# Optimization experiments

Hardware: AMD Instinct MI355X
Metric: run time of the kernel (lower is better)

Reference implementation:

```python
import jax, jax.numpy as jnp
import numpy as np

N_NODES, N_EDGES = 50000, 400000
D_IN, D_HID, D_OUT, N_LAYERS = 256, 512, 128, 4


def setup_inputs() -> dict:
    key = jax.random.key(0)
    ks = jax.random.split(key, 8)
    x = jax.random.normal(ks[0], (N_NODES, D_IN), jnp.float32)
    edge_index = jax.random.randint(ks[1], (2, N_EDGES), 0, N_NODES)
    # dnn1: Linear(D_IN, D_HID)
    W1 = jax.random.normal(ks[2], (D_IN, D_HID), jnp.float32) / np.sqrt(D_IN)
    b1 = jnp.zeros((D_HID,), jnp.float32)
    # stacked GCNConv weights: [L, D_HID, D_HID]
    Wc = jax.random.normal(ks[3], (N_LAYERS, D_HID, D_HID), jnp.float32) / np.sqrt(D_HID)
    bc = jnp.zeros((N_LAYERS, D_HID), jnp.float32)
    # dnn2: Linear(D_HID, D_OUT)
    W2 = jax.random.normal(ks[4], (D_HID, D_OUT), jnp.float32) / np.sqrt(D_HID)
    b2 = jnp.zeros((D_OUT,), jnp.float32)
    return {"x": x, "edge_index": edge_index, "W1": W1, "b1": b1,
            "Wc": Wc, "bc": bc, "W2": W2, "b2": b2}


def reference(x, edge_index, W1, b1, Wc, bc, W2, b2):
    N = x.shape[0]
    L = Wc.shape[0]
    # GCNConv: add self-loops once (same graph every layer)
    loops = jnp.arange(N, dtype=edge_index.dtype)
    src = jnp.concatenate([edge_index[0], loops])  # message sources
    dst = jnp.concatenate([edge_index[1], loops])  # message targets
    deg = jax.ops.segment_sum(jnp.ones_like(dst, dtype=x.dtype), dst, num_segments=N)
    dinv = jnp.where(deg > 0, jax.lax.rsqrt(deg), 0.0)  # deg >= 1 due to self-loops
    norm = dinv[src] * dinv[dst]                        # [E+N]

    # dnn1: Linear + ReLU
    h = jax.nn.relu(x @ W1 + b1)

    # GCN layers: h' = scatter_dst( norm * (h W)[src] ) + b
    for i in range(L):
        hw = h @ Wc[i]
        msgs = norm[:, None] * hw[src]                  # [E+N, D_HID]
        h = jax.ops.segment_sum(msgs, dst, num_segments=N) + bc[i]

    # dnn2: Linear
    return h @ W2 + b2
```

## Files before the change

kernel.cpp:

```cpp
#include <hip/hip_runtime.h>

typedef __bf16 bf16_t;
typedef __bf16 bf16x8 __attribute__((ext_vector_type(8)));
typedef float f32x4 __attribute__((ext_vector_type(4)));
typedef float f32x2 __attribute__((ext_vector_type(2)));

#define N_NODES 50000
#define N_PAD   50048
#define N_EDGES 400000
#define D_IN    256
#define D_HID   512
#define D_OUT   128
#define N_LAYERS 4
#define ZROW    N_PAD
#define CSR_CAP (N_EDGES + 3 * N_NODES + 64)
#define PZ_FLOATS (3 * 512 * 512)

#define AS1 __attribute__((address_space(1)))
#define AS3 __attribute__((address_space(3)))


__global__ void init_misc(int* __restrict__ deg, int* __restrict__ cursor,
                          int* __restrict__ csr_src, float* __restrict__ dinv,
                          float* __restrict__ u0, float* __restrict__ u1,
                          float* __restrict__ u2, bf16_t* __restrict__ FA,
                          bf16_t* __restrict__ FB, float* __restrict__ Pz) {
    int idx = blockIdx.x * blockDim.x + threadIdx.x;
    if (idx < CSR_CAP) csr_src[idx] = ZROW;
    if (idx < N_NODES) { deg[idx] = 0; cursor[idx] = 0; }
    if (idx < N_PAD - N_NODES) dinv[N_NODES + idx] = 0.0f;
    if (idx < N_PAD + 1 - N_NODES) {
        u0[N_NODES + idx] = 0.0f; u1[N_NODES + idx] = 0.0f; u2[N_NODES + idx] = 0.0f;
    }
    if (idx < 64) {
        ((unsigned*)(FA + (size_t)ZROW * D_OUT))[idx] = 0u;
        ((unsigned*)(FB + (size_t)ZROW * D_OUT))[idx] = 0u;
    }
    if (idx < PZ_FLOATS) Pz[idx] = 0.0f;
}


__global__ void f32_to_bf16(const float* __restrict__ in, bf16_t* __restrict__ out, int n) {
    int idx = (blockIdx.x * blockDim.x + threadIdx.x) * 4;
    if (idx + 3 < n) {
        float4 v = *reinterpret_cast<const float4*>(in + idx);
        bf16_t o[4] = {(bf16_t)v.x, (bf16_t)v.y, (bf16_t)v.z, (bf16_t)v.w};
        *reinterpret_cast<uint2*>(out + idx) = *reinterpret_cast<const uint2*>(o);
    } else {
        for (int j = idx; j < n; j++) out[j] = (bf16_t)in[j];
    }
}


__global__ void transpose_all(const float* __restrict__ W1, const float* __restrict__ Wc,
                              const float* __restrict__ W2, bf16_t* __restrict__ W1t,
                              float* __restrict__ W2cT, float* __restrict__ W4cT,
                              float* __restrict__ W2T) {
    const float* in; int R, C; bf16_t* outb = nullptr; float* outf = nullptr;
    const int z = blockIdx.z;
    if (z == 0)      { in = W1; R = D_IN;  C = D_HID; outb = W1t; }
    else if (z == 1) { in = Wc + (size_t)1 * D_HID * D_HID; R = D_HID; C = D_HID; outf = W2cT; }
    else if (z == 2) { in = Wc + (size_t)3 * D_HID * D_HID; R = D_HID; C = D_HID; outf = W4cT; }
    else             { in = W2; R = D_HID; C = D_OUT; outf = W2T; }

    const int c0 = blockIdx.x * 32;
    const int r0 = blockIdx.y * 32;
    if (c0 >= C || r0 >= R) return;
    __shared__ float tile[32][33];
    for (int i = threadIdx.y; i < 32; i += 8)
        tile[i][threadIdx.x] = in[(size_t)(r0 + i) * C + c0 + threadIdx.x];
    __syncthreads();
    for (int i = threadIdx.y; i < 32; i += 8) {
        if (outb) outb[(size_t)(c0 + i) * R + r0 + threadIdx.x] = (bf16_t)tile[threadIdx.x][i];
        else      outf[(size_t)(c0 + i) * R + r0 + threadIdx.x] = tile[threadIdx.x][i];
    }
}


__global__ void count_deg(const int* __restrict__ dst, int* __restrict__ deg, int E) {
    int e = blockIdx.x * blockDim.x + threadIdx.x;
    if (e < E) atomicAdd(&deg[dst[e]], 1);
}

__global__ void scan_reduce(const int* __restrict__ deg, int* __restrict__ partial, int N) {
    __shared__ int red[256];
    int base = blockIdx.x * 1024;
    int s = 0;
    for (int i = threadIdx.x; i < 1024; i += 256) {
        int idx = base + i;
        s += (idx < N) ? ((deg[idx] + 3) & ~3) : 0;
    }
    red[threadIdx.x] = s;
    __syncthreads();
    for (int off = 128; off > 0; off >>= 1) {
        if (threadIdx.x < off) red[threadIdx.x] += red[threadIdx.x + off];
        __syncthreads();
    }
    if (threadIdx.x == 0) partial[blockIdx.x] = red[0];
}

__global__ void scan_partials(int* __restrict__ partial, int nb,
                              int* __restrict__ row_start, int N) {
    if (threadIdx.x == 0 && blockIdx.x == 0) {
        int acc = 0;
        for (int i = 0; i < nb; i++) { int v = partial[i]; partial[i] = acc; acc += v; }
        row_start[N] = acc;
    }
}

__global__ void scan_chunks(const int* __restrict__ deg, const int* __restrict__ partial,
                            int* __restrict__ row_start, float* __restrict__ dinv,
                            float* __restrict__ u0, int N) {
    __shared__ int buf[2][1024];
    int t = threadIdx.x;
    int gid = blockIdx.x * 1024 + t;
    int d = (gid < N) ? deg[gid] : 0;
    int v = (gid < N) ? ((d + 3) & ~3) : 0;
    int cur = 0;
    buf[0][t] = v;
    __syncthreads();
    for (int off = 1; off < 1024; off <<= 1) {
        int nxt = cur ^ 1;
        int val = buf[cur][t];
        if (t >= off) val += buf[cur][t - off];
        buf[nxt][t] = val;
        cur = nxt;
        __syncthreads();
    }
    int incl = buf[cur][t];
    if (gid < N) {
        row_start[gid] = partial[blockIdx.x] + incl - v;
        float dv = rsqrtf((float)(d + 1));
        dinv[gid] = dv;
        u0[gid] = dv;
    }
}

__global__ void fill_csr(const int* __restrict__ ei, int E,
                         const int* __restrict__ row_start,
                         int* __restrict__ cursor, int* __restrict__ csr_src) {
    int e = blockIdx.x * blockDim.x + threadIdx.x;
    if (e < E) {
        int s = ei[e];
        int d = ei[E + e];
        int pos = atomicAdd(&cursor[d], 1);
        csr_src[row_start[d] + pos] = s;
    }
}


template <bool F32OUT, bool RELU>
__global__ __launch_bounds__(256, 4) void gemm_tile(
    const bf16_t* __restrict__ A, const bf16_t* __restrict__ BT,
    const float* __restrict__ bias, const float* __restrict__ rowscale,
    void* __restrict__ Cv, int M, int N, int K)
{
    __shared__ __align__(16) char smem[32768];
    bf16_t* sA = (bf16_t*)smem;
    bf16_t* sB = (bf16_t*)(smem + 128 * 128);
    bf16_t* sC = (bf16_t*)smem;

    int bxi, byi;
    if (gridDim.x == 4) {
        const int bid = blockIdx.y * 4 + blockIdx.x;
        const int T0 = (int)(gridDim.y * 4) & ~31;
        if (bid < T0) { int q = bid >> 5, r = bid & 31; byi = q * 8 + (r & 7); bxi = r >> 3; }
        else          { int t = bid - T0; byi = (T0 >> 2) + (t >> 2); bxi = t & 3; }
    } else { bxi = blockIdx.x; byi = blockIdx.y; }

    const int tid  = threadIdx.x;
    const int lane = tid & 63;
    const int wave = tid >> 6;
    const int bn = bxi * 128;
    const int bm = byi * 128;
    const int wm = (wave & 1) * 64;
    const int wn = (wave >> 1) * 64;
    const int lm = lane & 15;
    const int lq = lane >> 4;

    const int r8 = lane >> 3;
    const int c8 = lane & 7;
    const int ksw = (c8 ^ r8) * 8;

    f32x4 acc[4][4] = {};

    const int nkb = K >> 6;
    for (int kb = 0; kb < nkb; kb++) {
        const int k0 = kb * 64;
#pragma unroll
        for (int r = 0; r < 4; r++) {
            const int g = r * 4 + wave;
            __builtin_amdgcn_global_load_lds(
                (const AS1 unsigned int*)(A + (size_t)(bm + g * 8 + r8) * K + k0 + ksw),
                (AS3 unsigned int*)((AS3 char*)(AS3 bf16_t*)sA + g * 1024),
                16, 0, 0);
        }
#pragma unroll
        for (int r = 0; r < 4; r++) {
            const int g = r * 4 + wave;
            __builtin_amdgcn_global_load_lds(
                (const AS1 unsigned int*)(BT + (size_t)(bn + g * 8 + r8) * K + k0 + ksw),
                (AS3 unsigned int*)((AS3 char*)(AS3 bf16_t*)sB + g * 1024),
                16, 0, 0);
        }
        __syncthreads();

#pragma unroll
        for (int s = 0; s < 2; s++) {
            bf16x8 af[4], bfr[4];
#pragma unroll
            for (int mt = 0; mt < 4; mt++) {
                const int R = wm + mt * 16 + lm;
                const int g = s * 4 + lq;
                af[mt] = *reinterpret_cast<bf16x8*>(&sA[R * 64 + ((g ^ (R & 7)) * 8)]);
            }
#pragma unroll
            for (int nt = 0; nt < 4; nt++) {
                const int R = wn + nt * 16 + lm;
                const int g = s * 4 + lq;
                bfr[nt] = *reinterpret_cast<bf16x8*>(&sB[R * 64 + ((g ^ (R & 7)) * 8)]);
            }
#pragma unroll
            for (int mt = 0; mt < 4; mt++)
#pragma unroll
                for (int nt = 0; nt < 4; nt++)
                    acc[mt][nt] = __builtin_amdgcn_mfma_f32_16x16x32_bf16(af[mt], bfr[nt], acc[mt][nt], 0, 0, 0);
        }
        __syncthreads();
    }

    if (!F32OUT) {
        const size_t rowbytes = (size_t)N * 2;
#pragma unroll
        for (int p = 0; p < 2; p++) {
            if (p) __syncthreads();
            if ((wave & 1) == p) {
#pragma unroll
                for (int nt = 0; nt < 4; nt++) {
                    const int col = wn + nt * 16 + lm;
                    const float bv = bias ? bias[bn + col] : 0.0f;
#pragma unroll
                    for (int mt = 0; mt < 4; mt++) {
#pragma unroll
                        for (int r = 0; r < 4; r++) {
                            const int lrow = mt * 16 + lq * 4 + r;
                            float v = acc[mt][nt][r] + bv;
                            if (rowscale) v *= rowscale[bm + p * 64 + lrow];
                            if (RELU) v = fmaxf(v, 0.0f);
                            sC[lrow * 136 + col] = (bf16_t)v;
                        }
                    }
                }
            }
            __syncthreads();
            char* outbase = (char*)Cv + (size_t)(bm + p * 64) * rowbytes + (size_t)bn * 2;
#pragma unroll
            for (int j = 0; j < 4; j++) {
                const int idx = j * 4096 + tid * 16;
                const int row = idx >> 8;
                const int colb = idx & 255;
                *reinterpret_cast<uint4*>(outbase + (size_t)row * rowbytes + colb) =
                    *reinterpret_cast<const uint4*>((char*)sC + (size_t)row * 272 + colb);
            }
        }
    } else {
#pragma unroll
        for (int nt = 0; nt < 4; nt++) {
            const int col = bn + wn + nt * 16 + lm;
            const float bv = bias ? bias[col] : 0.0f;
#pragma unroll
            for (int mt = 0; mt < 4; mt++) {
#pragma unroll
                for (int r = 0; r < 4; r++) {
                    const int row = bm + wm + mt * 16 + lq * 4 + r;
                    if (row < M) {
                        float v = acc[mt][nt][r] + bv;
                        if (rowscale) v *= rowscale[row];
                        if (RELU) v = fmaxf(v, 0.0f);
                        ((float*)Cv)[(size_t)row * N + col] = v;
                    }
                }
            }
        }
    }
}


__global__ __launch_bounds__(256) void mm3(
    const float* __restrict__ A0, const float* __restrict__ B0, float* __restrict__ C0,
    const float* __restrict__ A1, const float* __restrict__ B1, float* __restrict__ C1,
    bf16_t* __restrict__ Cb, int M, int N, int K, int kc, int outmode)
{
    int z = blockIdx.z;
    const float* A = A0; const float* BT = B0; float* C = C0;
    if (z >= kc) { A = A1; BT = B1; C = C1; z -= kc; }
    const int n0 = blockIdx.x * 64;
    const int m0 = blockIdx.y * 64;
    const int lane = threadIdx.x & 63;
    const int w    = threadIdx.x >> 6;
    const int lm = lane & 15, lq = lane >> 4;
    const int klen = K / kc;
    const int kbeg = z * klen;
    const int arow = m0 + w * 16 + lm;

    f32x4 acc[4] = {};
    for (int k = kbeg; k < kbeg + klen; k += 32) {
        const float* ap = A + (size_t)arow * K + k + lq * 8;
        float4 av0 = *reinterpret_cast<const float4*>(ap);
        float4 av1 = *reinterpret_cast<const float4*>(ap + 4);
        float av[8] = {av0.x, av0.y, av0.z, av0.w, av1.x, av1.y, av1.z, av1.w};
        bf16x8 ah, al;
#pragma unroll
        for (int j = 0; j < 8; j++) {
            bf16_t h = (bf16_t)av[j]; ah[j] = h; al[j] = (bf16_t)(av[j] - (float)h);
        }
#pragma unroll
        for (int nt = 0; nt < 4; nt++) {
            const float* bp = BT + (size_t)(n0 + nt * 16 + lm) * K + k + lq * 8;
            float4 bv0 = *reinterpret_cast<const float4*>(bp);
            float4 bv1 = *reinterpret_cast<const float4*>(bp + 4);
            float bv[8] = {bv0.x, bv0.y, bv0.z, bv0.w, bv1.x, bv1.y, bv1.z, bv1.w};
            bf16x8 bh, bl;
#pragma unroll
            for (int j = 0; j < 8; j++) {
                bf16_t h = (bf16_t)bv[j]; bh[j] = h; bl[j] = (bf16_t)(bv[j] - (float)h);
            }
            acc[nt] = __builtin_amdgcn_mfma_f32_16x16x32_bf16(ah, bh, acc[nt], 0, 0, 0);
            acc[nt] = __builtin_amdgcn_mfma_f32_16x16x32_bf16(al, bh, acc[nt], 0, 0, 0);
            acc[nt] = __builtin_amdgcn_mfma_f32_16x16x32_bf16(ah, bl, acc[nt], 0, 0, 0);
        }
    }
#pragma unroll
    for (int nt = 0; nt < 4; nt++) {
#pragma unroll
        for (int r = 0; r < 4; r++) {
            const int row = m0 + w * 16 + lq * 4 + r;
            const int col = n0 + nt * 16 + lm;
            if (outmode == 0) atomicAdd(&C[(size_t)row * N + col], acc[nt][r]);
            else              Cb[(size_t)row * N + col] = (bf16_t)acc[nt][r];
        }
    }
}


__global__ void vstep(const float* __restrict__ Vin, const float* __restrict__ W,
                      float* __restrict__ Vout, int rcnt, int Ncols,
                      const float* __restrict__ addb) {
    const int r = threadIdx.x >> 6;
    const int c = blockIdx.x * 64 + (threadIdx.x & 63);
    if (r < rcnt) {
        float acc = 0.0f;
        for (int k = 0; k < D_HID; k++) acc += Vin[r * D_HID + k] * W[(size_t)k * Ncols + c];
        if (addb && r == 3) acc += addb[c];
        Vout[r * Ncols + c] = acc;
    } else {
        Vout[r * Ncols + c] = Vin[r * D_HID + c];
    }
}


__global__ void s_agg(const float* __restrict__ uin, const float* __restrict__ dinv,
                      const int* __restrict__ row_start, const int* __restrict__ csr_src,
                      float* __restrict__ sout, float* __restrict__ uout, int N)
{
    int n = blockIdx.x * blockDim.x + threadIdx.x;
    if (n >= N) return;
    float a = uin[n];
    const int beg = row_start[n], end = row_start[n + 1];
    for (int i = beg; i < end; i++) a += uin[csr_src[i]];
    const float sv = dinv[n] * a;
    sout[n] = sv;
    uout[n] = dinv[n] * sv;
}


template <bool FINAL>
__global__ __launch_bounds__(256) void agg128(
    const bf16_t* __restrict__ tin, const float* __restrict__ dinv,
    const int* __restrict__ row_start, const int* __restrict__ csr_src,
    bf16_t* __restrict__ tout, float* __restrict__ fout,
    const float* __restrict__ s1, const float* __restrict__ s2,
    const float* __restrict__ s3, const float* __restrict__ cvec, int N)
{
    const int n = blockIdx.x * 4 + (threadIdx.x >> 6);
    const int lane = threadIdx.x & 63;
    if (n >= N) return;
    const float dn = dinv[n];
    const char* tb = (const char*)tin + lane * 4;

    f32x2 acc;
    {
        unsigned u = *reinterpret_cast<const unsigned*>(tb + ((size_t)n << 8));
        acc[0] = __uint_as_float(u << 16);
        acc[1] = __uint_as_float(u & 0xffff0000u);
    }
    const int beg = row_start[n];
    const int cnt = row_start[n + 1] - beg;
    const int* ip = csr_src + beg;

    int i = 0;
    for (; i + 8 <= cnt; i += 8) {
        const int4 a = *reinterpret_cast<const int4*>(ip + i);
        const int4 b = *reinterpret_cast<const int4*>(ip + i + 4);
        unsigned u[8];
        u[0] = *reinterpret_cast<const unsigned*>(tb + ((size_t)a.x << 8));
        u[1] = *reinterpret_cast<const unsigned*>(tb + ((size_t)a.y << 8));
        u[2] = *reinterpret_cast<const unsigned*>(tb + ((size_t)a.z << 8));
        u[3] = *reinterpret_cast<const unsigned*>(tb + ((size_t)a.w << 8));
        u[4] = *reinterpret_cast<const unsigned*>(tb + ((size_t)b.x << 8));
        u[5] = *reinterpret_cast<const unsigned*>(tb + ((size_t)b.y << 8));
        u[6] = *reinterpret_cast<const unsigned*>(tb + ((size_t)b.z << 8));
        u[7] = *reinterpret_cast<const unsigned*>(tb + ((size_t)b.w << 8));
#pragma unroll
        for (int q = 0; q < 8; q++) {
            acc[0] += __uint_as_float(u[q] << 16);
            acc[1] += __uint_as_float(u[q] & 0xffff0000u);
        }
    }
    if (i < cnt) {
        const int4 a = *reinterpret_cast<const int4*>(ip + i);
        unsigned u[4];
        u[0] = *reinterpret_cast<const unsigned*>(tb + ((size_t)a.x << 8));
        u[1] = *reinterpret_cast<const unsigned*>(tb + ((size_t)a.y << 8));
        u[2] = *reinterpret_cast<const unsigned*>(tb + ((size_t)a.z << 8));
        u[3] = *reinterpret_cast<const unsigned*>(tb + ((size_t)a.w << 8));
#pragma unroll
        for (int q = 0; q < 4; q++) {
            acc[0] += __uint_as_float(u[q] << 16);
            acc[1] += __uint_as_float(u[q] & 0xffff0000u);
        }
    }

    if (!FINAL) {
        const float sc = dn * dn;
        bf16_t o2[2] = {(bf16_t)(sc * acc[0]), (bf16_t)(sc * acc[1])};
        *reinterpret_cast<unsigned*>((char*)tout + ((size_t)n << 8) + lane * 4) =
            *reinterpret_cast<const unsigned*>(o2);
    } else {
        const int f = lane * 2;
        const float w3 = s3[n], w2 = s2[n], w1 = s1[n];
        float o0 = dn * acc[0] + w3 * cvec[f]     + w2 * cvec[128 + f]
                 + w1 * cvec[256 + f]     + cvec[384 + f];
        float o1 = dn * acc[1] + w3 * cvec[f + 1] + w2 * cvec[128 + f + 1]
                 + w1 * cvec[256 + f + 1] + cvec[384 + f + 1];
        float2 ov = make_float2(o0, o1);
        *reinterpret_cast<float2*>(fout + (size_t)n * D_OUT + f) = ov;
    }
}


extern "C" void kernel_launch(void* const* d_in, const int* in_sizes, int n_in,
                              void* d_out, int out_size, void* d_ws, size_t ws_size,
                              hipStream_t stream) {
    const int N = N_NODES, E = N_EDGES;
    const size_t DD = (size_t)D_HID * D_HID;

    const float* x  = (const float*)d_in[0];
    const int*   ei = (const int*)d_in[1];
    const float* W1 = (const float*)d_in[2];
    const float* b1 = (const float*)d_in[3];
    const float* Wc = (const float*)d_in[4];
    const float* bc = (const float*)d_in[5];
    const float* W2 = (const float*)d_in[6];
    const float* b2 = (const float*)d_in[7];
    float* out = (float*)d_out;

    char* ws = (char*)d_ws;
    size_t off = 0;
    auto alloc = [&](size_t bytes) -> void* {
        void* p = ws + off;
        off += (bytes + 255) & ~(size_t)255;
        return p;
    };
    int*    deg       = (int*)alloc((size_t)N * 4);
    int*    cursor    = (int*)alloc((size_t)N * 4);
    int*    row_start = (int*)alloc((size_t)(N + 1) * 4);
    int*    partial   = (int*)alloc(256 * 4);
    float*  dinv      = (float*)alloc((size_t)N_PAD * 4);
    float*  u0        = (float*)alloc((size_t)(N_PAD + 1) * 4);
    float*  u1        = (float*)alloc((size_t)(N_PAD + 1) * 4);
    float*  u2        = (float*)alloc((size_t)(N_PAD + 1) * 4);
    float*  s1        = (float*)alloc((size_t)N * 4);
    float*  s2        = (float*)alloc((size_t)N * 4);
    float*  s3        = (float*)alloc((size_t)N * 4);
    int*    csr_src   = (int*)alloc((size_t)CSR_CAP * 4);
    bf16_t* xb        = (bf16_t*)alloc((size_t)N_PAD * D_IN * 2);
    bf16_t* h0        = (bf16_t*)alloc((size_t)N_PAD * D_HID * 2);
    bf16_t* FA        = (bf16_t*)alloc((size_t)(N_PAD + 1) * D_OUT * 2);
    bf16_t* FB        = (bf16_t*)alloc((size_t)(N_PAD + 1) * D_OUT * 2);
    bf16_t* W1t       = (bf16_t*)alloc((size_t)D_HID * D_IN * 2);
    float*  W2cT      = (float*)alloc(DD * 4);
    float*  W4cT      = (float*)alloc(DD * 4);
    float*  W2T       = (float*)alloc((size_t)D_OUT * D_HID * 4);
    float*  Pz        = (float*)alloc(3 * DD * 4);
    float*  P12 = Pz, *Q = Pz + DD, *P = Pz + 2 * DD;
    bf16_t* WbigT     = (bf16_t*)alloc((size_t)D_OUT * D_HID * 2);
    float*  V0        = (float*)alloc(4 * 512 * 4);
    float*  V1        = (float*)alloc(4 * 512 * 4);
    float*  cvec      = (float*)alloc(4 * 128 * 4);

    init_misc<<<(PZ_FLOATS + 255) / 256, 256, 0, stream>>>(
        deg, cursor, csr_src, dinv, u0, u1, u2, FA, FB, Pz);

    {
        int n = N * D_IN;
        f32_to_bf16<<<(n / 4 + 255) / 256, 256, 0, stream>>>(x, xb, n);
        transpose_all<<<dim3(16, 16, 4), dim3(32, 8), 0, stream>>>(
            W1, Wc, W2, W1t, W2cT, W4cT, W2T);
    }

    count_deg<<<(E + 255) / 256, 256, 0, stream>>>(ei + E, deg, E);
    const int nch = (N + 1023) / 1024;
    scan_reduce<<<nch, 256, 0, stream>>>(deg, partial, N);
    scan_partials<<<1, 64, 0, stream>>>(partial, nch, row_start, N);
    scan_chunks<<<nch, 1024, 0, stream>>>(deg, partial, row_start, dinv, u0, N);
    fill_csr<<<(E + 255) / 256, 256, 0, stream>>>(ei, E, row_start, cursor, csr_src);

    mm3<<<dim3(8, 8, 8), 256, 0, stream>>>(
        Wc, W2cT, P12,
        W4cT, Wc + 2 * DD, Q,
        nullptr, 512, 512, 512, 4, 0);
    mm3<<<dim3(8, 8, 4), 256, 0, stream>>>(
        P12, Q, P, P12, Q, P, nullptr, 512, 512, 512, 4, 0);
    mm3<<<dim3(8, 2, 1), 256, 0, stream>>>(
        W2T, P, P, W2T, P, P, WbigT, 128, 512, 512, 1, 1);

    vstep<<<8, 256, 0, stream>>>(bc, Wc + DD,     V0,   1, 512, nullptr);
    vstep<<<8, 256, 0, stream>>>(V0, Wc + 2 * DD, V1,   2, 512, nullptr);
    vstep<<<8, 256, 0, stream>>>(V1, Wc + 3 * DD, V0,   3, 512, nullptr);
    vstep<<<2, 256, 0, stream>>>(V0, W2,          cvec, 4, 128, b2);

    s_agg<<<(N + 255) / 256, 256, 0, stream>>>(u0, dinv, row_start, csr_src, s1, u1, N);
    s_agg<<<(N + 255) / 256, 256, 0, stream>>>(u1, dinv, row_start, csr_src, s2, u2, N);
    s_agg<<<(N + 255) / 256, 256, 0, stream>>>(u2, dinv, row_start, csr_src, s3, u1, N);

    const dim3 blk(256);
    const int mg = N_PAD / 128;

    gemm_tile<false, true><<<dim3(4, mg), blk, 0, stream>>>(
        xb, W1t, b1, nullptr, h0, N_PAD, D_HID, D_IN);

    gemm_tile<false, false><<<dim3(1, mg), blk, 0, stream>>>(
        h0, WbigT, nullptr, dinv, FA, N_PAD, D_OUT, D_HID);

    const int ag = (N + 3) / 4;
    agg128<false><<<ag, blk, 0, stream>>>(FA, dinv, row_start, csr_src, FB, nullptr,
                                          nullptr, nullptr, nullptr, nullptr, N);
    agg128<false><<<ag, blk, 0, stream>>>(FB, dinv, row_start, csr_src, FA, nullptr,
                                          nullptr, nullptr, nullptr, nullptr, N);
    agg128<false><<<ag, blk, 0, stream>>>(FA, dinv, row_start, csr_src, FB, nullptr,
                                          nullptr, nullptr, nullptr, nullptr, N);
    agg128<true><<<ag, blk, 0, stream>>>(FB, dinv, row_start, csr_src, nullptr, out,
                                         s1, s2, s3, cvec, N);
}
```

Before: 529.8 us.

## Fuse init with x conversion, merge bias chain, widen agg128 gathers

Merges the init kernel and the fp32-to-bf16 conversion of x into one launch, and replaces four vstep launches with a single-block bias_chain kernel that keeps the intermediate vectors in shared memory. agg128 now splits each wavefront into four 16-lane groups that each gather full 256-byte rows with 16-byte loads across different edges, then reduces across groups with shuffles. The aim is fewer launches and fewer, wider memory transactions in the aggregation. The cost is that bias_chain runs serially on one block, and the shuffle reduction adds work per node.

Result: slower. 551.6 us (+4.1%).

```diff
diff --git a/kernel.cpp b/kernel.cpp
--- a/kernel.cpp
+++ b/kernel.cpp
@@ -20,11 +20,13 @@
 #define AS3 __attribute__((address_space(3)))
 
 
-__global__ void init_misc(int* __restrict__ deg, int* __restrict__ cursor,
-                          int* __restrict__ csr_src, float* __restrict__ dinv,
-                          float* __restrict__ u0, float* __restrict__ u1,
-                          float* __restrict__ u2, bf16_t* __restrict__ FA,
-                          bf16_t* __restrict__ FB, float* __restrict__ Pz) {
+__global__ void init_convert(int* __restrict__ deg, int* __restrict__ cursor,
+                             int* __restrict__ csr_src, float* __restrict__ dinv,
+                             float* __restrict__ u0, float* __restrict__ u1,
+                             float* __restrict__ u2, bf16_t* __restrict__ FA,
+                             bf16_t* __restrict__ FB, float* __restrict__ Pz,
+                             const float* __restrict__ x, bf16_t* __restrict__ xb,
+                             int nconv) {
     int idx = blockIdx.x * blockDim.x + threadIdx.x;
     if (idx < CSR_CAP) csr_src[idx] = ZROW;
     if (idx < N_NODES) { deg[idx] = 0; cursor[idx] = 0; }
@@ -37,17 +39,11 @@
         ((unsigned*)(FB + (size_t)ZROW * D_OUT))[idx] = 0u;
     }
     if (idx < PZ_FLOATS) Pz[idx] = 0.0f;
-}
-
-
-__global__ void f32_to_bf16(const float* __restrict__ in, bf16_t* __restrict__ out, int n) {
-    int idx = (blockIdx.x * blockDim.x + threadIdx.x) * 4;
-    if (idx + 3 < n) {
-        float4 v = *reinterpret_cast<const float4*>(in + idx);
+    const int c4 = idx * 4;
+    if (c4 + 3 < nconv) {
+        float4 v = *reinterpret_cast<const float4*>(x + c4);
         bf16_t o[4] = {(bf16_t)v.x, (bf16_t)v.y, (bf16_t)v.z, (bf16_t)v.w};
-        *reinterpret_cast<uint2*>(out + idx) = *reinterpret_cast<const uint2*>(o);
-    } else {
-        for (int j = idx; j < n; j++) out[j] = (bf16_t)in[j];
+        *reinterpret_cast<uint2*>(xb + c4) = *reinterpret_cast<const uint2*>(o);
     }
 }
 
@@ -343,18 +339,45 @@
 }
 
 
-__global__ void vstep(const float* __restrict__ Vin, const float* __restrict__ W,
-                      float* __restrict__ Vout, int rcnt, int Ncols,
-                      const float* __restrict__ addb) {
-    const int r = threadIdx.x >> 6;
-    const int c = blockIdx.x * 64 + (threadIdx.x & 63);
-    if (r < rcnt) {
-        float acc = 0.0f;
-        for (int k = 0; k < D_HID; k++) acc += Vin[r * D_HID + k] * W[(size_t)k * Ncols + c];
-        if (addb && r == 3) acc += addb[c];
-        Vout[r * Ncols + c] = acc;
-    } else {
-        Vout[r * Ncols + c] = Vin[r * D_HID + c];
+__global__ __launch_bounds__(256) void bias_chain(
+    const float* __restrict__ bc, const float* __restrict__ Wc,
+    const float* __restrict__ W2, const float* __restrict__ b2,
+    float* __restrict__ cvec)
+{
+    __shared__ float V[4][512];
+    const int t = threadIdx.x;
+#pragma unroll
+    for (int r = 0; r < 4; r++) {
+        V[r][t] = bc[r * 512 + t];
+        V[r][t + 256] = bc[r * 512 + t + 256];
+    }
+    __syncthreads();
+    for (int j = 0; j < 3; j++) {
+        const float* W = Wc + (size_t)(j + 1) * 512 * 512;
+        float nv[3][2];
+        for (int r = 0; r <= j; r++) {
+            float a0 = 0.0f, a1 = 0.0f;
+#pragma unroll 8
+            for (int k = 0; k < 512; k++) {
+                const float vk = V[r][k];
+                a0 += vk * W[(size_t)k * 512 + t];
+                a1 += vk * W[(size_t)k * 512 + t + 256];
+            }
+            nv[r][0] = a0; nv[r][1] = a1;
+        }
+        __syncthreads();
+        for (int r = 0; r <= j; r++) { V[r][t] = nv[r][0]; V[r][t + 256] = nv[r][1]; }
+        __syncthreads();
+    }
+    if (t < 128) {
+#pragma unroll
+        for (int r = 0; r < 4; r++) {
+            float a = 0.0f;
+#pragma unroll 8
+            for (int k = 0; k < 512; k++) a += V[r][k] * W2[(size_t)k * 128 + t];
+            if (r == 3) a += b2[t];
+            cvec[r * 128 + t] = a;
+        }
     }
 }
 
@@ -374,6 +397,15 @@
 }
 
 
+#define UNP4(accv, uvec) do {                                         \
+    const unsigned* _w = reinterpret_cast<const unsigned*>(&(uvec));  \
+    _Pragma("unroll")                                                 \
+    for (int _j = 0; _j < 4; _j++) {                                  \
+        (accv)[_j][0] += __uint_as_float(_w[_j] << 16);               \
+        (accv)[_j][1] += __uint_as_float(_w[_j] & 0xffff0000u);       \
+    }                                                                 \
+} while (0)
+
 template <bool FINAL>
 __global__ __launch_bounds__(256) void agg128(
     const bf16_t* __restrict__ tin, const float* __restrict__ dinv,
@@ -385,66 +417,81 @@
     const int n = blockIdx.x * 4 + (threadIdx.x >> 6);
     const int lane = threadIdx.x & 63;
     if (n >= N) return;
-    const float dn = dinv[n];
-    const char* tb = (const char*)tin + lane * 4;
-
-    f32x2 acc;
-    {
-        unsigned u = *reinterpret_cast<const unsigned*>(tb + ((size_t)n << 8));
-        acc[0] = __uint_as_float(u << 16);
-        acc[1] = __uint_as_float(u & 0xffff0000u);
-    }
+    const int g  = lane >> 4;
+    const int fl = lane & 15;
+    const char* tb = (const char*)tin + fl * 16;
+
+    f32x2 acc[4] = {};
+    if (g == 0) {
+        uint4 u = *reinterpret_cast<const uint4*>(tb + ((size_t)n << 8));
+        UNP4(acc, u);
+    }
+
     const int beg = row_start[n];
     const int cnt = row_start[n + 1] - beg;
-    const int* ip = csr_src + beg;
+    const int* ip = csr_src + beg + g;
 
     int i = 0;
-    for (; i + 8 <= cnt; i += 8) {
-        const int4 a = *reinterpret_cast<const int4*>(ip + i);
-        const int4 b = *reinterpret_cast<const int4*>(ip + i + 4);
-        unsigned u[8];
-        u[0] = *reinterpret_cast<const unsigned*>(tb + ((size_t)a.x << 8));
-        u[1] = *reinterpret_cast<const unsigned*>(tb + ((size_t)a.y << 8));
-        u[2] = *reinterpret_cast<const unsigned*>(tb + ((size_t)a.z << 8));
-        u[3] = *reinterpret_cast<const unsigned*>(tb + ((size_t)a.w << 8));
-        u[4] = *reinterpret_cast<const unsigned*>(tb + ((size_t)b.x << 8));
-        u[5] = *reinterpret_cast<const unsigned*>(tb + ((size_t)b.y << 8));
-        u[6] = *reinterpret_cast<const unsigned*>(tb + ((size_t)b.z << 8));
-        u[7] = *reinterpret_cast<const unsigned*>(tb + ((size_t)b.w << 8));
-#pragma unroll
-        for (int q = 0; q < 8; q++) {
-            acc[0] += __uint_as_float(u[q] << 16);
-            acc[1] += __uint_as_float(u[q] & 0xffff0000u);
-        }
+    for (; i + 16 <= cnt; i += 16) {
+        const int sa = ip[i], sb = ip[i + 4], sc = ip[i + 8], sd = ip[i + 12];
+        uint4 u0 = *reinterpret_cast<const uint4*>(tb + ((size_t)sa << 8));
+        uint4 u1 = *reinterpret_cast<const uint4*>(tb + ((size_t)sb << 8));
+        uint4 u2 = *reinterpret_cast<const uint4*>(tb + ((size_t)sc << 8));
+        uint4 u3 = *reinterpret_cast<const uint4*>(tb + ((size_t)sd << 8));
+        UNP4(acc, u0); UNP4(acc, u1); UNP4(acc, u2); UNP4(acc, u3);
+    }
+    if (i + 8 <= cnt) {
+        const int sa = ip[i], sb = ip[i + 4];
+        uint4 u0 = *reinterpret_cast<const uint4*>(tb + ((size_t)sa << 8));
+        uint4 u1 = *reinterpret_cast<const uint4*>(tb + ((size_t)sb << 8));
+        UNP4(acc, u0); UNP4(acc, u1);
+        i += 8;
     }
     if (i < cnt) {
-        const int4 a = *reinterpret_cast<const int4*>(ip + i);
-        unsigned u[4];
-        u[0] = *reinterpret_cast<const unsigned*>(tb + ((size_t)a.x << 8));
-        u[1] = *reinterpret_cast<const unsigned*>(tb + ((size_t)a.y << 8));
-        u[2] = *reinterpret_cast<const unsigned*>(tb + ((size_t)a.z << 8));
-        u[3] = *reinterpret_cast<const unsigned*>(tb + ((size_t)a.w << 8));
-#pragma unroll
-        for (int q = 0; q < 4; q++) {
-            acc[0] += __uint_as_float(u[q] << 16);
-            acc[1] += __uint_as_float(u[q] & 0xffff0000u);
-        }
-    }
-
+        const int sa = ip[i];
+        uint4 u0 = *reinterpret_cast<const uint4*>(tb + ((size_t)sa << 8));
+        UNP4(acc, u0);
+    }
+
+#pragma unroll
+    for (int j = 0; j < 4; j++) {
+        acc[j][0] += __shfl_xor(acc[j][0], 16);
+        acc[j][0] += __shfl_xor(acc[j][0], 32);
+        acc[j][1] += __shfl_xor(acc[j][1], 16);
+        acc[j][1] += __shfl_xor(acc[j][1], 32);
+    }
+
+    const float dn = dinv[n];
     if (!FINAL) {
-        const float sc = dn * dn;
-        bf16_t o2[2] = {(bf16_t)(sc * acc[0]), (bf16_t)(sc * acc[1])};
-        *reinterpret_cast<unsigned*>((char*)tout + ((size_t)n << 8) + lane * 4) =
-            *reinterpret_cast<const unsigned*>(o2);
+        if (g == 0) {
+            const float sc = dn * dn;
+            bf16_t o[8];
+#pragma unroll
+            for (int j = 0; j < 4; j++) {
+                o[2 * j]     = (bf16_t)(sc * acc[j][0]);
+                o[2 * j + 1] = (bf16_t)(sc * acc[j][1]);
+            }
+            *reinterpret_cast<uint4*>((char*)tout + ((size_t)n << 8) + fl * 16) =
+                *reinterpret_cast<const uint4*>(o);
+        }
     } else {
-        const int f = lane * 2;
-        const float w3 = s3[n], w2 = s2[n], w1 = s1[n];
-        float o0 = dn * acc[0] + w3 * cvec[f]     + w2 * cvec[128 + f]
-                 + w1 * cvec[256 + f]     + cvec[384 + f];
-        float o1 = dn * acc[1] + w3 * cvec[f + 1] + w2 * cvec[128 + f + 1]
-                 + w1 * cvec[256 + f + 1] + cvec[384 + f + 1];
-        float2 ov = make_float2(o0, o1);
-        *reinterpret_cast<float2*>(fout + (size_t)n * D_OUT + f) = ov;
+        if (g == 0) {
+            const int f = fl * 8;
+            const float w3 = s3[n], w2 = s2[n], w1 = s1[n];
+            float o[8];
+#pragma unroll
+            for (int j = 0; j < 4; j++) {
+                o[2 * j]     = dn * acc[j][0];
+                o[2 * j + 1] = dn * acc[j][1];
+            }
+#pragma unroll
+            for (int j = 0; j < 8; j++)
+                o[j] += w3 * cvec[f + j] + w2 * cvec[128 + f + j]
+                      + w1 * cvec[256 + f + j] + cvec[384 + f + j];
+            float* op = fout + (size_t)n * D_OUT + f;
+            *reinterpret_cast<float4*>(op)     = make_float4(o[0], o[1], o[2], o[3]);
+            *reinterpret_cast<float4*>(op + 4) = make_float4(o[4], o[5], o[6], o[7]);
+        }
     }
 }
 
@@ -495,19 +542,16 @@
     float*  Pz        = (float*)alloc(3 * DD * 4);
     float*  P12 = Pz, *Q = Pz + DD, *P = Pz + 2 * DD;
     bf16_t* WbigT     = (bf16_t*)alloc((size_t)D_OUT * D_HID * 2);
-    float*  V0        = (float*)alloc(4 * 512 * 4);
-    float*  V1        = (float*)alloc(4 * 512 * 4);
     float*  cvec      = (float*)alloc(4 * 128 * 4);
 
-    init_misc<<<(PZ_FLOATS + 255) / 256, 256, 0, stream>>>(
-        deg, cursor, csr_src, dinv, u0, u1, u2, FA, FB, Pz);
-
     {
-        int n = N * D_IN;
-        f32_to_bf16<<<(n / 4 + 255) / 256, 256, 0, stream>>>(x, xb, n);
-        transpose_all<<<dim3(16, 16, 4), dim3(32, 8), 0, stream>>>(
-            W1, Wc, W2, W1t, W2cT, W4cT, W2T);
-    }
+        const int nconv = N * D_IN;
+        const int nthreads = nconv / 4;
+        init_convert<<<(nthreads + 255) / 256, 256, 0, stream>>>(
+            deg, cursor, csr_src, dinv, u0, u1, u2, FA, FB, Pz, x, xb, nconv);
+    }
+    transpose_all<<<dim3(16, 16, 4), dim3(32, 8), 0, stream>>>(
+        W1, Wc, W2, W1t, W2cT, W4cT, W2T);
 
     count_deg<<<(E + 255) / 256, 256, 0, stream>>>(ei + E, deg, E);
     const int nch = (N + 1023) / 1024;
@@ -525,10 +569,7 @@
     mm3<<<dim3(8, 2, 1), 256, 0, stream>>>(
         W2T, P, P, W2T, P, P, WbigT, 128, 512, 512, 1, 1);
 
-    vstep<<<8, 256, 0, stream>>>(bc, Wc + DD,     V0,   1, 512, nullptr);
-    vstep<<<8, 256, 0, stream>>>(V0, Wc + 2 * DD, V1,   2, 512, nullptr);
-    vstep<<<8, 256, 0, stream>>>(V1, Wc + 3 * DD, V0,   3, 512, nullptr);
-    vstep<<<2, 256, 0, stream>>>(V0, W2,          cvec, 4, 128, b2);
+    bias_chain<<<1, 256, 0, stream>>>(bc, Wc, W2, b2, cvec);
 
     s_agg<<<(N + 255) / 256, 256, 0, stream>>>(u0, dinv, row_start, csr_src, s1, u1, N);
     s_agg<<<(N + 255) / 256, 256, 0, stream>>>(u1, dinv, row_start, csr_src, s2, u2, N);
```
